# Kernel optimization log

Hardware: AMD Instinct MI355X
Metric: run time of the kernel (lower is better)

Reference implementation:

```python
import jax, jax.numpy as jnp
import numpy as np

N_JOINTS, JOINT_DIM, TIMESTEPS = 24, 3, 120
BATCH = 16384


def setup_inputs() -> dict:
    key = jax.random.key(0)
    k1, k2 = jax.random.split(key)
    src = jax.random.normal(k1, (BATCH, N_JOINTS * JOINT_DIM, TIMESTEPS), dtype=jnp.float32)
    tgt = jax.random.normal(k2, (BATCH, N_JOINTS * JOINT_DIM, TIMESTEPS), dtype=jnp.float32)
    return {"src": src, "tgt": tgt}


def reference(src, tgt):
    # Original while-loop computes, for every (joint n, timestep t),
    # torch.linalg.norm(src[:, 3n:3n+3, t] - tgt[:, 3n:3n+3, t])  (Frobenius over [B, 3]),
    # and sums all J*T norms into a scalar.
    B = src.shape[0]
    diff = (src - tgt).reshape(B, N_JOINTS, JOINT_DIM, TIMESTEPS)
    sq = jnp.sum(diff * diff, axis=(0, 2))  # [J, T]: sum of squares over batch & joint_dim
    return jnp.sum(jnp.sqrt(sq))
```

## Files before the change

### kernel.cpp

```cpp
#include <hip/hip_runtime.h>
#include <math.h>

#define NJ   24
#define JD   3
#define TS   120
#define B_TOT 16384
#define CT   (NJ * JD * TS)
#define CT4  (CT / 4)
#define NCHUNK 128
#define BPC  (B_TOT / NCHUNK)

__global__ void pj_zero(float* __restrict__ sq) {
    int i = blockIdx.x * blockDim.x + threadIdx.x;
    if (i < CT) sq[i] = 0.0f;
}

__global__ void pj_accum(const float* __restrict__ src,
                         const float* __restrict__ tgt,
                         float* __restrict__ sq) {
    int p4 = blockIdx.x * blockDim.x + threadIdx.x;
    if (p4 >= CT4) return;
    const float4* s = (const float4*)src;
    const float4* t = (const float4*)tgt;
    long base = (long)blockIdx.y * BPC * CT4 + p4;
    float ax = 0.f, ay = 0.f, az = 0.f, aw = 0.f;
    #pragma unroll 4
    for (int b = 0; b < BPC; ++b) {
        float4 a = s[base];
        float4 c = t[base];
        float dx = a.x - c.x, dy = a.y - c.y, dz = a.z - c.z, dw = a.w - c.w;
        ax += dx * dx; ay += dy * dy; az += dz * dz; aw += dw * dw;
        base += CT4;
    }
    atomicAdd(&sq[p4 * 4 + 0], ax);
    atomicAdd(&sq[p4 * 4 + 1], ay);
    atomicAdd(&sq[p4 * 4 + 2], az);
    atomicAdd(&sq[p4 * 4 + 3], aw);
}

__global__ void pj_finalize(const float* __restrict__ sq, float* __restrict__ out) {
    float local = 0.0f;
    for (int i = threadIdx.x; i < NJ * TS; i += blockDim.x) {
        int n = i / TS, t = i - (i / TS) * TS;
        float s = sq[(3 * n + 0) * TS + t]
                + sq[(3 * n + 1) * TS + t]
                + sq[(3 * n + 2) * TS + t];
        local += sqrtf(s);
    }
    for (int off = 32; off > 0; off >>= 1)
        local += __shfl_down(local, off, 64);
    __shared__ float red[4];
    int lane = threadIdx.x & 63, wid = threadIdx.x >> 6;
    if (lane == 0) red[wid] = local;
    __syncthreads();
    if (threadIdx.x == 0) {
        float tot = 0.f;
        int nw = blockDim.x >> 6;
        for (int w = 0; w < nw; ++w) tot += red[w];
        out[0] = tot;
    }
}

extern "C" void kernel_launch(void* const* d_in, const int* in_sizes, int n_in,
                              void* d_out, int out_size, void* d_ws, size_t ws_size,
                              hipStream_t stream) {
    const float* src = (const float*)d_in[0];
    const float* tgt = (const float*)d_in[1];
    float* sq = (float*)d_ws;
    float* out = (float*)d_out;

    pj_zero<<<(CT + 255) / 256, 256, 0, stream>>>(sq);

    dim3 grid((CT4 + 255) / 256, NCHUNK);
    pj_accum<<<grid, 256, 0, stream>>>(src, tgt, sq);

    pj_finalize<<<1, 256, 0, stream>>>(sq, out);
}
```

Measured before the change: 217.3 us.

## Stream contiguous batch rows per block with LDS atomic accumulation and two-stage reduction

```diff
diff --git a/kernel.cpp b/kernel.cpp
--- a/kernel.cpp
+++ b/kernel.cpp
@@ -1,64 +1,80 @@
 #include <hip/hip_runtime.h>
 #include <math.h>
 
-#define NJ   24
-#define JD   3
-#define TS   120
+#define NJ 24
+#define JD 3
+#define TS 120
 #define B_TOT 16384
-#define CT   (NJ * JD * TS)
-#define CT4  (CT / 4)
-#define NCHUNK 128
-#define BPC  (B_TOT / NCHUNK)
+#define ROWF 8640
+#define ROWP 2160
+#define BROWS 16
+#define NBLK (B_TOT / BROWS)
+#define KTOT (BROWS * ROWP)
+#define CELLS (NJ * TS)
+#define S1CH 16
+#define S1B (NBLK / S1CH)
 
-__global__ void pj_zero(float* __restrict__ sq) {
-    int i = blockIdx.x * blockDim.x + threadIdx.x;
-    if (i < CT) sq[i] = 0.0f;
+__global__ __launch_bounds__(256, 4) void pj_accum(const float* __restrict__ src,
+                                                   const float* __restrict__ tgt,
+                                                   float* __restrict__ gpart) {
+    __shared__ float acc[4 * ROWP];
+    int tid = threadIdx.x;
+    for (int i = tid; i < 4 * ROWP; i += 256) acc[i] = 0.0f;
+    __syncthreads();
+
+    const float4* s = (const float4*)src;
+    const float4* t = (const float4*)tgt;
+    long base = (long)blockIdx.x * KTOT;
+    int p = tid;
+    #pragma unroll 5
+    for (int k = tid; k < KTOT; k += 256) {
+        float4 a = s[base + k];
+        float4 c = t[base + k];
+        float dx = a.x - c.x, dy = a.y - c.y, dz = a.z - c.z, dw = a.w - c.w;
+        atomicAdd(&acc[0 * ROWP + p], dx * dx);
+        atomicAdd(&acc[1 * ROWP + p], dy * dy);
+        atomicAdd(&acc[2 * ROWP + p], dz * dz);
+        atomicAdd(&acc[3 * ROWP + p], dw * dw);
+        p += 256;
+        p = (p >= ROWP) ? p - ROWP : p;
+    }
+    __syncthreads();
+
+    float* gp = gpart + (long)blockIdx.x * CELLS;
+    for (int cell = tid; cell < CELLS; cell += 256) {
+        int n = cell / TS, tt = cell - n * TS;
+        int b0 = (tt & 3) * ROWP + (tt >> 2);
+        float ssum = acc[b0 + (3 * n + 0) * 30]
+                   + acc[b0 + (3 * n + 1) * 30]
+                   + acc[b0 + (3 * n + 2) * 30];
+        gp[cell] = ssum;
+    }
 }
 
-__global__ void pj_accum(const float* __restrict__ src,
-                         const float* __restrict__ tgt,
-                         float* __restrict__ sq) {
-    int p4 = blockIdx.x * blockDim.x + threadIdx.x;
-    if (p4 >= CT4) return;
-    const float4* s = (const float4*)src;
-    const float4* t = (const float4*)tgt;
-    long base = (long)blockIdx.y * BPC * CT4 + p4;
-    float ax = 0.f, ay = 0.f, az = 0.f, aw = 0.f;
+__global__ void pj_reduce1(const float* __restrict__ gpart, float* __restrict__ gpart2) {
+    int cell = blockIdx.x * blockDim.x + threadIdx.x;
+    if (cell >= CELLS) return;
+    const float* gp = gpart + (long)blockIdx.y * S1B * CELLS + cell;
+    float sum = 0.f;
     #pragma unroll 4
-    for (int b = 0; b < BPC; ++b) {
-        float4 a = s[base];
-        float4 c = t[base];
-        float dx = a.x - c.x, dy = a.y - c.y, dz = a.z - c.z, dw = a.w - c.w;
-        ax += dx * dx; ay += dy * dy; az += dz * dz; aw += dw * dw;
-        base += CT4;
-    }
-    atomicAdd(&sq[p4 * 4 + 0], ax);
-    atomicAdd(&sq[p4 * 4 + 1], ay);
-    atomicAdd(&sq[p4 * 4 + 2], az);
-    atomicAdd(&sq[p4 * 4 + 3], aw);
+    for (int b = 0; b < S1B; ++b) sum += gp[(long)b * CELLS];
+    gpart2[blockIdx.y * CELLS + cell] = sum;
 }
 
-__global__ void pj_finalize(const float* __restrict__ sq, float* __restrict__ out) {
-    float local = 0.0f;
-    for (int i = threadIdx.x; i < NJ * TS; i += blockDim.x) {
-        int n = i / TS, t = i - (i / TS) * TS;
-        float s = sq[(3 * n + 0) * TS + t]
-                + sq[(3 * n + 1) * TS + t]
-                + sq[(3 * n + 2) * TS + t];
+__global__ void pj_reduce2(const float* __restrict__ gpart2, float* __restrict__ out) {
+    float local = 0.f;
+    for (int cell = threadIdx.x; cell < CELLS; cell += 256) {
+        float s = 0.f;
+        #pragma unroll
+        for (int g = 0; g < S1CH; ++g) s += gpart2[g * CELLS + cell];
         local += sqrtf(s);
     }
-    for (int off = 32; off > 0; off >>= 1)
-        local += __shfl_down(local, off, 64);
+    for (int off = 32; off > 0; off >>= 1) local += __shfl_down(local, off, 64);
     __shared__ float red[4];
     int lane = threadIdx.x & 63, wid = threadIdx.x >> 6;
     if (lane == 0) red[wid] = local;
     __syncthreads();
-    if (threadIdx.x == 0) {
-        float tot = 0.f;
-        int nw = blockDim.x >> 6;
-        for (int w = 0; w < nw; ++w) tot += red[w];
-        out[0] = tot;
-    }
+    if (threadIdx.x == 0) out[0] = red[0] + red[1] + red[2] + red[3];
 }
 
 extern "C" void kernel_launch(void* const* d_in, const int* in_sizes, int n_in,
@@ -66,13 +82,11 @@
                               hipStream_t stream) {
     const float* src = (const float*)d_in[0];
     const float* tgt = (const float*)d_in[1];
-    float* sq = (float*)d_ws;
+    float* gpart  = (float*)d_ws;
+    float* gpart2 = gpart + (long)NBLK * CELLS;
     float* out = (float*)d_out;
 
-    pj_zero<<<(CT + 255) / 256, 256, 0, stream>>>(sq);
-
-    dim3 grid((CT4 + 255) / 256, NCHUNK);
-    pj_accum<<<grid, 256, 0, stream>>>(src, tgt, sq);
-
-    pj_finalize<<<1, 256, 0, stream>>>(sq, out);
+    pj_accum<<<NBLK, 256, 0, stream>>>(src, tgt, gpart);
+    pj_reduce1<<<dim3(12, S1CH), 256, 0, stream>>>(gpart, gpart2);
+    pj_reduce2<<<1, 256, 0, stream>>>(gpart2, out);
 }
```

Result: slower. 730.4 us (+236.1%).
